# Performance work log

Hardware: AMD Instinct MI355X
Metric: run time of the kernel (lower is better)

## Reference

```python
import jax, jax.numpy as jnp
import numpy as np

N, N1, N2, K = 65536, 16384, 8192, 16
INDIM, HID, OUT = 64, 32, 128


def _knn_np(pos, q, k, chunk=1024):
    # brute-force chunked KNN (indices into pos) for setup only
    out = []
    for s in range(0, q.shape[0], chunk):
        d = ((q[s:s + chunk, None, :] - pos[None, :, :]) ** 2).sum(-1)
        out.append(np.argpartition(d, k, axis=1)[:, :k])
    return np.concatenate(out, 0)


def setup_inputs() -> dict:
    key = jax.random.key(0)
    ks = jax.random.split(key, 12)
    x = jax.random.normal(ks[0], (N, INDIM), jnp.float32)
    pos = jax.random.uniform(ks[1], (N, 3), jnp.float32)

    pos_np = np.asarray(pos)
    rng = np.random.default_rng(0)
    idx1 = np.sort(rng.choice(N, N1, replace=False))            # RandomSampler(ratio1)
    nn1 = _knn_np(pos_np, pos_np[idx1], K)                      # [N1, K] into full cloud
    src1, dst1 = nn1.reshape(-1), np.repeat(np.arange(N1), K)
    pos1 = pos_np[idx1]
    idx2 = np.sort(rng.choice(N1, N2, replace=False))           # RandomSampler(ratio2)
    nn2 = _knn_np(pos1, pos1[idx2], K)                          # [N2, K] into level-1 cloud
    src2, dst2 = nn2.reshape(-1), np.repeat(np.arange(N2), K)

    def lin(k, i, o):
        return jax.random.normal(k, (i, o), jnp.float32) / float(np.sqrt(i))

    return dict(
        x=x, pos=pos,
        W_down=lin(ks[2], INDIM, HID), b_down=jnp.zeros((HID,), jnp.float32),
        W_pp1=lin(ks[3], 10, 32), b_pp1=jnp.zeros((32,), jnp.float32),
        W_att1=lin(ks[4], 64, 64), b_att1=jnp.zeros((64,), jnp.float32),
        W_g1=lin(ks[5], 64, 64), b_g1=jnp.zeros((64,), jnp.float32),
        W_pp2=lin(ks[6], 10, 64), b_pp2=jnp.zeros((64,), jnp.float32),
        W_att2=lin(ks[7], 128, 128), b_att2=jnp.zeros((128,), jnp.float32),
        W_g2=lin(ks[8], 128, 128), b_g2=jnp.zeros((128,), jnp.float32),
        W_up=lin(ks[9], 128, OUT), b_up=jnp.zeros((OUT,), jnp.float32),
        W_sc=lin(ks[10], INDIM, OUT), b_sc=jnp.zeros((OUT,), jnp.float32),
        idx1=jnp.asarray(idx1, jnp.int32), idx2=jnp.asarray(idx2, jnp.int32),
        src1=jnp.asarray(src1, jnp.int32), dst1=jnp.asarray(dst1, jnp.int32),
        src2=jnp.asarray(src2, jnp.int32), dst2=jnp.asarray(dst2, jnp.int32),
    )


def _mlp(h, W, b):
    return jax.nn.relu(h @ W + b)


def _randla_conv(x, pos_all, pos_q, src, dst, Wpp, bpp, Watt, batt, Wg, bg, n_out):
    # RandlaKernel.message + add-aggregate + update (bipartite: targets = sampled points)
    pos_i, pos_j = pos_q[dst], pos_all[src]                     # [E,3]
    vij = pos_i - pos_j
    dij = jnp.sqrt((vij * vij).sum(-1, keepdims=True))          # [E,1]
    rel = jnp.concatenate([pos_i, pos_j, vij, dij], axis=1)     # [E,10]
    rij = _mlp(rel, Wpp, bpp)                                   # point_pos_nn
    fij = jnp.concatenate([x[src], rij], axis=1)                # [E, c+d]
    s = jax.nn.softmax(_mlp(fij, Watt, batt), axis=-1)          # softmax over feature dim (as in source)
    agg = jax.ops.segment_sum(s * fij, dst, num_segments=n_out) # aggr='add'
    return _mlp(agg, Wg, bg)                                    # global_nn


def reference(x, pos, W_down, b_down, W_pp1, b_pp1, W_att1, b_att1, W_g1, b_g1,
              W_pp2, b_pp2, W_att2, b_att2, W_g2, b_g2, W_up, b_up, W_sc, b_sc,
              idx1, idx2, src1, dst1, src2, dst2):
    h = _mlp(x, W_down, b_down)                                 # features_downsample (indim -> outdim//4)
    pos1 = pos[idx1]
    h = _randla_conv(h, pos, pos1, src1, dst1, W_pp1, b_pp1, W_att1, b_att1, W_g1, b_g1, N1)
    pos2 = pos1[idx2]
    h = _randla_conv(h, pos1, pos2, src2, dst2, W_pp2, b_pp2, W_att2, b_att2, W_g2, b_g2, N2)
    h = _mlp(h, W_up, b_up)                                     # features_upsample
    sc = _mlp(x[idx1][idx2], W_sc, b_sc)                        # shortcut resized, idx = idx1[idx2]
    return jax.nn.relu(h + sc)
```

## Files before the change

kernel.cpp:

```cpp
#include <hip/hip_runtime.h>

#define N_FULL 65536
#define NN1    16384
#define NN2    8192

typedef __attribute__((ext_vector_type(8))) short bf16x8;
typedef __attribute__((ext_vector_type(4))) float f32x4;
typedef unsigned short ushortT;

#define MFMA16(acc, a, b) acc = __builtin_amdgcn_mfma_f32_16x16x32_bf16(a, b, acc, 0, 0, 0)

static __device__ __forceinline__ ushortT f2bf(float f) {
    union { float f; unsigned u; } v; v.f = f;
    unsigned r = v.u + 0x7FFFu + ((v.u >> 16) & 1u);
    return (ushortT)(r >> 16);
}
static __device__ __forceinline__ unsigned pack2(float a, float b) {
    return (unsigned)f2bf(a) | ((unsigned)f2bf(b) << 16);
}
static __device__ __forceinline__ float bfu2f(ushortT h) {
    union { unsigned u; float f; } v; v.u = (unsigned)h << 16; return v.f;
}

#define WS_WDT   0
#define WS_WAT1  2304
#define WS_WGT1  6912
#define WS_WAT2  11520
#define WS_WGT2  28928
#define WS_WUPT  46336
#define WS_WSCT  63744
#define WS_H0    73728
#define WS_H1    (WS_H0 + 65536u*32u)
#define WS_AGG1  (WS_H1 + 16384u*64u)
#define WS_AGG2  (WS_AGG1 + 16384u*64u)

static __device__ __forceinline__ void tpose(
    const float* __restrict__ src, ushortT* __restrict__ dst,
    int K, int N, int STR, int gid, int gs)
{
    for (int i = gid; i < K * N; i += gs) {
        const int n = i / K, k = i - n * K;
        dst[n * STR + k] = f2bf(src[(size_t)k * N + n]);
    }
}

__global__ __launch_bounds__(256) void k_prep(
    const float* __restrict__ Wd, const float* __restrict__ Wa1,
    const float* __restrict__ Wg1, const float* __restrict__ Wa2,
    const float* __restrict__ Wg2, const float* __restrict__ Wup,
    const float* __restrict__ Wsc, ushortT* __restrict__ wsw)
{
    const int gid = blockIdx.x * 256 + threadIdx.x, gs = gridDim.x * 256;
    tpose(Wd,  wsw + WS_WDT,  64, 32, 72,  gid, gs);
    tpose(Wa1, wsw + WS_WAT1, 64, 64, 72,  gid, gs);
    tpose(Wg1, wsw + WS_WGT1, 64, 64, 72,  gid, gs);
    tpose(Wa2, wsw + WS_WAT2, 128, 128, 136, gid, gs);
    tpose(Wg2, wsw + WS_WGT2, 128, 128, 136, gid, gs);
    tpose(Wup, wsw + WS_WUPT, 128, 128, 136, gid, gs);
    tpose(Wsc, wsw + WS_WSCT, 64, 128, 72, gid, gs);
}

__global__ __launch_bounds__(256) void k_down(
    const float* __restrict__ x, const ushortT* __restrict__ wsw,
    const float* __restrict__ bd, ushortT* __restrict__ h0w)
{
    __shared__ ushortT Al[128 * 72];
    __shared__ ushortT Bl[32 * 72];
    const int t = threadIdx.x;
    const int rowBase = blockIdx.x * 128;

    {
        const int r = t >> 1, c0 = (t & 1) * 32;
        unsigned* dst = (unsigned*)Al + r * 36 + (c0 >> 1);
        const float* src = &x[(size_t)(rowBase + r) * 64 + c0];
#pragma unroll
        for (int j = 0; j < 32; j += 4) {
            const float4 v = *reinterpret_cast<const float4*>(src + j);
            dst[(j >> 1) + 0] = pack2(v.x, v.y);
            dst[(j >> 1) + 1] = pack2(v.z, v.w);
        }
        const unsigned* wsrc = (const unsigned*)(wsw + WS_WDT);
        for (int i = t; i < 1152; i += 256) ((unsigned*)Bl)[i] = wsrc[i];
    }
    __syncthreads();

    const int lane = t & 63, w = t >> 6, quad = lane >> 4, c16 = lane & 15;
    f32x4 acc[2][2];
#pragma unroll
    for (int mt = 0; mt < 2; ++mt)
#pragma unroll
        for (int nt = 0; nt < 2; ++nt)
#pragma unroll
            for (int r = 0; r < 4; ++r) acc[mt][nt][r] = 0.f;
#pragma unroll
    for (int ks = 0; ks < 2; ++ks) {
        bf16x8 a[2], b[2];
#pragma unroll
        for (int mt = 0; mt < 2; ++mt)
            a[mt] = *(const bf16x8*)&Al[(w * 32 + mt * 16 + c16) * 72 + ks * 32 + quad * 8];
#pragma unroll
        for (int nt = 0; nt < 2; ++nt)
            b[nt] = *(const bf16x8*)&Bl[(nt * 16 + c16) * 72 + ks * 32 + quad * 8];
#pragma unroll
        for (int mt = 0; mt < 2; ++mt)
#pragma unroll
            for (int nt = 0; nt < 2; ++nt) MFMA16(acc[mt][nt], a[mt], b[nt]);
    }
#pragma unroll
    for (int nt = 0; nt < 2; ++nt) {
        const int col = nt * 16 + c16;
        const float bias = bd[col];
#pragma unroll
        for (int mt = 0; mt < 2; ++mt)
#pragma unroll
            for (int r = 0; r < 4; ++r) {
                const int row = rowBase + w * 32 + mt * 16 + quad * 4 + r;
                h0w[(size_t)row * 32 + col] = f2bf(fmaxf(acc[mt][nt][r] + bias, 0.f));
            }
    }
}

__global__ __launch_bounds__(256) void k_conv1(
    const ushortT* __restrict__ h0w, const float* __restrict__ pos,
    const int* __restrict__ idx1, const int* __restrict__ src1,
    const float* __restrict__ Wpp, const float* __restrict__ bpp,
    const ushortT* __restrict__ wsw, const float* __restrict__ batt,
    ushortT* __restrict__ agg1w)
{
    __shared__ ushortT Fl[128 * 72];
    __shared__ ushortT Wl[64 * 72];
    __shared__ float Pl[352];
    const int t = threadIdx.x;
    const int d0 = blockIdx.x * 8;

    {
        const unsigned* wsrc = (const unsigned*)(wsw + WS_WAT1);
        for (int i = t; i < 2304; i += 256) ((unsigned*)Wl)[i] = wsrc[i];
        for (int i = t; i < 352; i += 256) Pl[i] = (i < 320) ? Wpp[i] : bpp[i - 320];
    }
    __syncthreads();

    {
        const int e = t >> 1, half = t & 1;
        const int g = e >> 4;
        const int s = src1[(d0 + g) * 16 + (e & 15)];
        const unsigned* srcp = (const unsigned*)h0w + (size_t)s * 16 + half * 8;
        unsigned* dstp = (unsigned*)Fl + e * 36 + half * 8;
#pragma unroll
        for (int j = 0; j < 8; ++j) dstp[j] = srcp[j];

        const int pin = idx1[d0 + g];
        const float pix = pos[pin * 3 + 0], piy = pos[pin * 3 + 1], piz = pos[pin * 3 + 2];
        const float pjx = pos[s * 3 + 0],  pjy = pos[s * 3 + 1],  pjz = pos[s * 3 + 2];
        const float vx = pix - pjx, vy = piy - pjy, vz = piz - pjz;
        const float dij = sqrtf(vx * vx + vy * vy + vz * vz);
        const float rel[10] = {pix, piy, piz, pjx, pjy, pjz, vx, vy, vz, dij};
        const int c0 = half * 16;
#pragma unroll
        for (int c = 0; c < 16; c += 2) {
            float a0 = Pl[320 + c0 + c], a1 = Pl[320 + c0 + c + 1];
#pragma unroll
            for (int i = 0; i < 10; ++i) {
                a0 += rel[i] * Pl[i * 32 + c0 + c];
                a1 += rel[i] * Pl[i * 32 + c0 + c + 1];
            }
            ((unsigned*)Fl)[(e * 72 + 32 + c0 + c) >> 1] = pack2(fmaxf(a0, 0.f), fmaxf(a1, 0.f));
        }
    }
    __syncthreads();

    const int lane = t & 63, w = t >> 6, quad = lane >> 4, c16 = lane & 15;
    f32x4 acc[2][4];
#pragma unroll
    for (int mt = 0; mt < 2; ++mt)
#pragma unroll
        for (int nt = 0; nt < 4; ++nt)
#pragma unroll
            for (int r = 0; r < 4; ++r) acc[mt][nt][r] = 0.f;
#pragma unroll
    for (int ks = 0; ks < 2; ++ks) {
        bf16x8 a[2], b[4];
#pragma unroll
        for (int mt = 0; mt < 2; ++mt)
            a[mt] = *(const bf16x8*)&Fl[(w * 32 + mt * 16 + c16) * 72 + ks * 32 + quad * 8];
#pragma unroll
        for (int nt = 0; nt < 4; ++nt)
            b[nt] = *(const bf16x8*)&Wl[(nt * 16 + c16) * 72 + ks * 32 + quad * 8];
#pragma unroll
        for (int mt = 0; mt < 2; ++mt)
#pragma unroll
            for (int nt = 0; nt < 4; ++nt) MFMA16(acc[mt][nt], a[mt], b[nt]);
    }
    float bcol[4];
#pragma unroll
    for (int nt = 0; nt < 4; ++nt) bcol[nt] = batt[nt * 16 + c16];

#pragma unroll
    for (int mt = 0; mt < 2; ++mt) {
#pragma unroll
        for (int nt = 0; nt < 4; ++nt)
#pragma unroll
            for (int r = 0; r < 4; ++r)
                acc[mt][nt][r] = fmaxf(acc[mt][nt][r] + bcol[nt], 0.f);
        float rs[4];
#pragma unroll
        for (int r = 0; r < 4; ++r) {
            float mx = acc[mt][0][r];
#pragma unroll
            for (int nt = 1; nt < 4; ++nt) mx = fmaxf(mx, acc[mt][nt][r]);
            mx = fmaxf(mx, __shfl_xor(mx, 1));
            mx = fmaxf(mx, __shfl_xor(mx, 2));
            mx = fmaxf(mx, __shfl_xor(mx, 4));
            mx = fmaxf(mx, __shfl_xor(mx, 8));
            float sm = 0.f;
#pragma unroll
            for (int nt = 0; nt < 4; ++nt) {
                acc[mt][nt][r] = __expf(acc[mt][nt][r] - mx);
                sm += acc[mt][nt][r];
            }
            sm += __shfl_xor(sm, 1);
            sm += __shfl_xor(sm, 2);
            sm += __shfl_xor(sm, 4);
            sm += __shfl_xor(sm, 8);
            rs[r] = 1.f / sm;
        }
#pragma unroll
        for (int nt = 0; nt < 4; ++nt) {
            float v = 0.f;
#pragma unroll
            for (int r = 0; r < 4; ++r) {
                const float fv = bfu2f(Fl[(w * 32 + mt * 16 + quad * 4 + r) * 72 + nt * 16 + c16]);
                v += acc[mt][nt][r] * rs[r] * fv;
            }
            v += __shfl_xor(v, 16);
            v += __shfl_xor(v, 32);
            if (lane < 16)
                agg1w[(size_t)(d0 + w * 2 + mt) * 64 + nt * 16 + c16] = f2bf(v);
        }
    }
}

__global__ __launch_bounds__(256) void k_gemm1(
    const ushortT* __restrict__ agg1w, const ushortT* __restrict__ wsw,
    const float* __restrict__ bg, ushortT* __restrict__ h1w)
{
    __shared__ ushortT Al[128 * 72];
    __shared__ ushortT Wl[64 * 72];
    const int t = threadIdx.x;
    const int d0 = blockIdx.x * 128;

    for (int i = t; i < 4096; i += 256) {
        const int r = i >> 5, j = i & 31;
        ((unsigned*)Al)[r * 36 + j] = ((const unsigned*)agg1w)[(size_t)(d0 + r) * 32 + j];
    }
    {
        const unsigned* wsrc = (const unsigned*)(wsw + WS_WGT1);
        for (int i = t; i < 2304; i += 256) ((unsigned*)Wl)[i] = wsrc[i];
    }
    __syncthreads();

    const int lane = t & 63, w = t >> 6, quad = lane >> 4, c16 = lane & 15;
    f32x4 acc[2][4];
#pragma unroll
    for (int mt = 0; mt < 2; ++mt)
#pragma unroll
        for (int nt = 0; nt < 4; ++nt)
#pragma unroll
            for (int r = 0; r < 4; ++r) acc[mt][nt][r] = 0.f;
#pragma unroll
    for (int ks = 0; ks < 2; ++ks) {
        bf16x8 a[2], b[4];
#pragma unroll
        for (int mt = 0; mt < 2; ++mt)
            a[mt] = *(const bf16x8*)&Al[(w * 32 + mt * 16 + c16) * 72 + ks * 32 + quad * 8];
#pragma unroll
        for (int nt = 0; nt < 4; ++nt)
            b[nt] = *(const bf16x8*)&Wl[(nt * 16 + c16) * 72 + ks * 32 + quad * 8];
#pragma unroll
        for (int mt = 0; mt < 2; ++mt)
#pragma unroll
            for (int nt = 0; nt < 4; ++nt) MFMA16(acc[mt][nt], a[mt], b[nt]);
    }
#pragma unroll
    for (int nt = 0; nt < 4; ++nt) {
        const int col = nt * 16 + c16;
        const float bias = bg[col];
#pragma unroll
        for (int mt = 0; mt < 2; ++mt)
#pragma unroll
            for (int r = 0; r < 4; ++r) {
                const int row = d0 + w * 32 + mt * 16 + quad * 4 + r;
                h1w[(size_t)row * 64 + col] = f2bf(fmaxf(acc[mt][nt][r] + bias, 0.f));
            }
    }
}

__global__ __launch_bounds__(256) void k_conv2(
    const ushortT* __restrict__ h1w, const float* __restrict__ pos,
    const int* __restrict__ idx1, const int* __restrict__ idx2,
    const int* __restrict__ src2,
    const float* __restrict__ Wpp, const float* __restrict__ bpp,
    const ushortT* __restrict__ wsw, const float* __restrict__ batt,
    ushortT* __restrict__ agg2w)
{
    __shared__ ushortT Fl[128 * 136];
    __shared__ ushortT Wl[128 * 136];
    __shared__ float Pl[704];
    const int t = threadIdx.x;
    const int d0 = blockIdx.x * 8;

    {
        const unsigned* wsrc = (const unsigned*)(wsw + WS_WAT2);
        for (int i = t; i < 8704; i += 256) ((unsigned*)Wl)[i] = wsrc[i];
        for (int i = t; i < 704; i += 256) Pl[i] = (i < 640) ? Wpp[i] : bpp[i - 640];
    }
    __syncthreads();

    {
        const int e = t >> 1, half = t & 1;
        const int g = e >> 4;
        const int s = src2[(d0 + g) * 16 + (e & 15)];
        const unsigned* srcp = (const unsigned*)h1w + (size_t)s * 32 + half * 16;
        unsigned* dstp = (unsigned*)Fl + e * 68 + half * 16;
#pragma unroll
        for (int j = 0; j < 16; ++j) dstp[j] = srcp[j];

        const int pin = idx1[idx2[d0 + g]];
        const int sn = idx1[s];
        const float pix = pos[pin * 3 + 0], piy = pos[pin * 3 + 1], piz = pos[pin * 3 + 2];
        const float pjx = pos[sn * 3 + 0],  pjy = pos[sn * 3 + 1],  pjz = pos[sn * 3 + 2];
        const float vx = pix - pjx, vy = piy - pjy, vz = piz - pjz;
        const float dij = sqrtf(vx * vx + vy * vy + vz * vz);
        const float rel[10] = {pix, piy, piz, pjx, pjy, pjz, vx, vy, vz, dij};
        const int c0 = half * 32;
#pragma unroll
        for (int c = 0; c < 32; c += 2) {
            float a0 = Pl[640 + c0 + c], a1 = Pl[640 + c0 + c + 1];
#pragma unroll
            for (int i = 0; i < 10; ++i) {
                a0 += rel[i] * Pl[i * 64 + c0 + c];
                a1 += rel[i] * Pl[i * 64 + c0 + c + 1];
            }
            ((unsigned*)Fl)[(e * 136 + 64 + c0 + c) >> 1] = pack2(fmaxf(a0, 0.f), fmaxf(a1, 0.f));
        }
    }
    __syncthreads();

    const int lane = t & 63, w = t >> 6, quad = lane >> 4, c16 = lane & 15;
    f32x4 acc[2][8];
#pragma unroll
    for (int mt = 0; mt < 2; ++mt)
#pragma unroll
        for (int nt = 0; nt < 8; ++nt)
#pragma unroll
            for (int r = 0; r < 4; ++r) acc[mt][nt][r] = 0.f;
#pragma unroll
    for (int ks = 0; ks < 4; ++ks) {
        bf16x8 a[2], b[8];
#pragma unroll
        for (int mt = 0; mt < 2; ++mt)
            a[mt] = *(const bf16x8*)&Fl[(w * 32 + mt * 16 + c16) * 136 + ks * 32 + quad * 8];
#pragma unroll
        for (int nt = 0; nt < 8; ++nt)
            b[nt] = *(const bf16x8*)&Wl[(nt * 16 + c16) * 136 + ks * 32 + quad * 8];
#pragma unroll
        for (int mt = 0; mt < 2; ++mt)
#pragma unroll
            for (int nt = 0; nt < 8; ++nt) MFMA16(acc[mt][nt], a[mt], b[nt]);
    }
    float bcol[8];
#pragma unroll
    for (int nt = 0; nt < 8; ++nt) bcol[nt] = batt[nt * 16 + c16];

#pragma unroll
    for (int mt = 0; mt < 2; ++mt) {
#pragma unroll
        for (int nt = 0; nt < 8; ++nt)
#pragma unroll
            for (int r = 0; r < 4; ++r)
                acc[mt][nt][r] = fmaxf(acc[mt][nt][r] + bcol[nt], 0.f);
        float rs[4];
#pragma unroll
        for (int r = 0; r < 4; ++r) {
            float mx = acc[mt][0][r];
#pragma unroll
            for (int nt = 1; nt < 8; ++nt) mx = fmaxf(mx, acc[mt][nt][r]);
            mx = fmaxf(mx, __shfl_xor(mx, 1));
            mx = fmaxf(mx, __shfl_xor(mx, 2));
            mx = fmaxf(mx, __shfl_xor(mx, 4));
            mx = fmaxf(mx, __shfl_xor(mx, 8));
            float sm = 0.f;
#pragma unroll
            for (int nt = 0; nt < 8; ++nt) {
                acc[mt][nt][r] = __expf(acc[mt][nt][r] - mx);
                sm += acc[mt][nt][r];
            }
            sm += __shfl_xor(sm, 1);
            sm += __shfl_xor(sm, 2);
            sm += __shfl_xor(sm, 4);
            sm += __shfl_xor(sm, 8);
            rs[r] = 1.f / sm;
        }
#pragma unroll
        for (int nt = 0; nt < 8; ++nt) {
            float v = 0.f;
#pragma unroll
            for (int r = 0; r < 4; ++r) {
                const float fv = bfu2f(Fl[(w * 32 + mt * 16 + quad * 4 + r) * 136 + nt * 16 + c16]);
                v += acc[mt][nt][r] * rs[r] * fv;
            }
            v += __shfl_xor(v, 16);
            v += __shfl_xor(v, 32);
            if (lane < 16)
                agg2w[(size_t)(d0 + w * 2 + mt) * 128 + nt * 16 + c16] = f2bf(v);
        }
    }
}

__global__ __launch_bounds__(256) void k_post(
    const ushortT* __restrict__ agg2w, const float* __restrict__ x,
    const int* __restrict__ idx1, const int* __restrict__ idx2,
    const ushortT* __restrict__ wsw,
    const float* __restrict__ bg, const float* __restrict__ bup,
    const float* __restrict__ bsc, float* __restrict__ out)
{
    __shared__ ushortT Al[64 * 136];
    __shared__ ushortT Wl[128 * 136];
    __shared__ ushortT Bl[64 * 136];
    __shared__ ushortT A2[64 * 72];
    const int t = threadIdx.x;
    const int d0 = blockIdx.x * 64;

    for (int i = t; i < 4096; i += 256) {
        const int r = i >> 6, j = i & 63;
        ((unsigned*)Al)[r * 68 + j] = ((const unsigned*)agg2w)[(size_t)(d0 + r) * 64 + j];
    }
    {
        const int r = t >> 2, q = t & 3;
        const int pin = idx1[idx2[d0 + r]];
        const float* src = &x[(size_t)pin * 64 + q * 16];
        unsigned* dst = (unsigned*)A2 + r * 36 + q * 8;
#pragma unroll
        for (int j = 0; j < 8; ++j) {
            const float2 v = *reinterpret_cast<const float2*>(src + j * 2);
            dst[j] = pack2(v.x, v.y);
        }
    }
    {
        const unsigned* wsrc = (const unsigned*)(wsw + WS_WGT2);
        for (int i = t; i < 8704; i += 256) ((unsigned*)Wl)[i] = wsrc[i];
    }
    __syncthreads();

    const int lane = t & 63, w = t >> 6, quad = lane >> 4, c16 = lane & 15;

    {
        f32x4 acc[8];
#pragma unroll
        for (int nt = 0; nt < 8; ++nt)
#pragma unroll
            for (int r = 0; r < 4; ++r) acc[nt][r] = 0.f;
#pragma unroll
        for (int ks = 0; ks < 4; ++ks) {
            const bf16x8 a = *(const bf16x8*)&Al[(w * 16 + c16) * 136 + ks * 32 + quad * 8];
#pragma unroll
            for (int nt = 0; nt < 8; ++nt) {
                const bf16x8 b = *(const bf16x8*)&Wl[(nt * 16 + c16) * 136 + ks * 32 + quad * 8];
                MFMA16(acc[nt], a, b);
            }
        }
#pragma unroll
        for (int nt = 0; nt < 8; ++nt) {
            const int col = nt * 16 + c16;
            const float bias = bg[col];
#pragma unroll
            for (int r = 0; r < 4; ++r)
                Bl[(w * 16 + quad * 4 + r) * 136 + col] = f2bf(fmaxf(acc[nt][r] + bias, 0.f));
        }
    }
    __syncthreads();
    {
        const unsigned* wsrc = (const unsigned*)(wsw + WS_WUPT);
        for (int i = t; i < 8704; i += 256) ((unsigned*)Wl)[i] = wsrc[i];
    }
    __syncthreads();

    f32x4 u[8];
    {
#pragma unroll
        for (int nt = 0; nt < 8; ++nt)
#pragma unroll
            for (int r = 0; r < 4; ++r) u[nt][r] = 0.f;
#pragma unroll
        for (int ks = 0; ks < 4; ++ks) {
            const bf16x8 a = *(const bf16x8*)&Bl[(w * 16 + c16) * 136 + ks * 32 + quad * 8];
#pragma unroll
            for (int nt = 0; nt < 8; ++nt) {
                const bf16x8 b = *(const bf16x8*)&Wl[(nt * 16 + c16) * 136 + ks * 32 + quad * 8];
                MFMA16(u[nt], a, b);
            }
        }
#pragma unroll
        for (int nt = 0; nt < 8; ++nt) {
            const float bias = bup[nt * 16 + c16];
#pragma unroll
            for (int r = 0; r < 4; ++r) u[nt][r] = fmaxf(u[nt][r] + bias, 0.f);
        }
    }
    __syncthreads();
    {
        const unsigned* wsrc = (const unsigned*)(wsw + WS_WSCT);
        for (int i = t; i < 4608; i += 256) ((unsigned*)Wl)[i] = wsrc[i];
    }
    __syncthreads();

    {
        f32x4 acc[8];
#pragma unroll
        for (int nt = 0; nt < 8; ++nt)
#pragma unroll
            for (int r = 0; r < 4; ++r) acc[nt][r] = 0.f;
        const ushortT* Wsc_l = Wl;
#pragma unroll
        for (int ks = 0; ks < 2; ++ks) {
            const bf16x8 a = *(const bf16x8*)&A2[(w * 16 + c16) * 72 + ks * 32 + quad * 8];
#pragma unroll
            for (int nt = 0; nt < 8; ++nt) {
                const bf16x8 b = *(const bf16x8*)&Wsc_l[(nt * 16 + c16) * 72 + ks * 32 + quad * 8];
                MFMA16(acc[nt], a, b);
            }
        }
#pragma unroll
        for (int nt = 0; nt < 8; ++nt) {
            const int col = nt * 16 + c16;
            const float bias = bsc[col];
#pragma unroll
            for (int r = 0; r < 4; ++r) {
                const float sc = fmaxf(acc[nt][r] + bias, 0.f);
                const int row = d0 + w * 16 + quad * 4 + r;
                out[(size_t)row * 128 + col] = u[nt][r] + sc;
            }
        }
    }
}

extern "C" void kernel_launch(void* const* d_in, const int* in_sizes, int n_in,
                              void* d_out, int out_size, void* d_ws, size_t ws_size,
                              hipStream_t stream)
{
    const float* x      = (const float*)d_in[0];
    const float* pos    = (const float*)d_in[1];
    const float* W_down = (const float*)d_in[2];
    const float* b_down = (const float*)d_in[3];
    const float* W_pp1  = (const float*)d_in[4];
    const float* b_pp1  = (const float*)d_in[5];
    const float* W_att1 = (const float*)d_in[6];
    const float* b_att1 = (const float*)d_in[7];
    const float* W_g1   = (const float*)d_in[8];
    const float* b_g1   = (const float*)d_in[9];
    const float* W_pp2  = (const float*)d_in[10];
    const float* b_pp2  = (const float*)d_in[11];
    const float* W_att2 = (const float*)d_in[12];
    const float* b_att2 = (const float*)d_in[13];
    const float* W_g2   = (const float*)d_in[14];
    const float* b_g2   = (const float*)d_in[15];
    const float* W_up   = (const float*)d_in[16];
    const float* b_up   = (const float*)d_in[17];
    const float* W_sc   = (const float*)d_in[18];
    const float* b_sc   = (const float*)d_in[19];
    const int* idx1 = (const int*)d_in[20];
    const int* idx2 = (const int*)d_in[21];
    const int* src1 = (const int*)d_in[22];
    const int* src2 = (const int*)d_in[24];

    ushortT* wsw = (ushortT*)d_ws;
    ushortT* h0w   = wsw + WS_H0;
    ushortT* h1w   = wsw + WS_H1;
    ushortT* agg1w = wsw + WS_AGG1;
    ushortT* agg2w = wsw + WS_AGG2;

    k_prep <<<68, 256, 0, stream>>>(W_down, W_att1, W_g1, W_att2, W_g2, W_up, W_sc, wsw);
    k_down <<<N_FULL / 128, 256, 0, stream>>>(x, wsw, b_down, h0w);
    k_conv1<<<NN1 / 8, 256, 0, stream>>>(h0w, pos, idx1, src1,
                                         W_pp1, b_pp1, wsw, b_att1, agg1w);
    k_gemm1<<<NN1 / 128, 256, 0, stream>>>(agg1w, wsw, b_g1, h1w);
    k_conv2<<<NN2 / 8, 256, 0, stream>>>(h1w, pos, idx1, idx2, src2,
                                         W_pp2, b_pp2, wsw, b_att2, agg2w);
    k_post <<<NN2 / 64, 256, 0, stream>>>(agg2w, x, idx1, idx2, wsw,
                                          b_g2, b_up, b_sc, (float*)d_out);
}
```

Before: 203.0 us.

## Fuse global_nn GEMM into conv1, vectorize loads, shrink post tiles

The level-1 global_nn GEMM moves into k_conv1: each block writes its 8 aggregated rows to a zero-padded 16-row LDS tile and applies W_g1 with one MFMA per wave. This removes the agg1 round trip through global memory and one kernel launch. Weight and gather copies are widened to uint4 loads. The sync after the weight loads is moved to overlap with the gather and position math. k_post is halved to 32 rows per block, giving more blocks but more redundant weight loads per row, and conv1 now uses extra LDS for W_g1.

```diff
diff --git a/kernel.cpp b/kernel.cpp
--- a/kernel.cpp
+++ b/kernel.cpp
@@ -31,8 +31,7 @@
 #define WS_WSCT  63744
 #define WS_H0    73728
 #define WS_H1    (WS_H0 + 65536u*32u)
-#define WS_AGG1  (WS_H1 + 16384u*64u)
-#define WS_AGG2  (WS_AGG1 + 16384u*64u)
+#define WS_AGG2  (WS_H1 + 16384u*64u)
 
 static __device__ __forceinline__ void tpose(
     const float* __restrict__ src, ushortT* __restrict__ dst,
@@ -64,8 +63,8 @@
     const float* __restrict__ x, const ushortT* __restrict__ wsw,
     const float* __restrict__ bd, ushortT* __restrict__ h0w)
 {
-    __shared__ ushortT Al[128 * 72];
-    __shared__ ushortT Bl[32 * 72];
+    __shared__ __align__(16) ushortT Al[128 * 72];
+    __shared__ __align__(16) ushortT Bl[32 * 72];
     const int t = threadIdx.x;
     const int rowBase = blockIdx.x * 128;
 
@@ -79,8 +78,9 @@
             dst[(j >> 1) + 0] = pack2(v.x, v.y);
             dst[(j >> 1) + 1] = pack2(v.z, v.w);
         }
-        const unsigned* wsrc = (const unsigned*)(wsw + WS_WDT);
-        for (int i = t; i < 1152; i += 256) ((unsigned*)Bl)[i] = wsrc[i];
+        const uint4* wsrc = (const uint4*)(wsw + WS_WDT);
+        uint4* bl4 = (uint4*)Bl;
+        for (int i = t; i < 288; i += 256) bl4[i] = wsrc[i];
     }
     __syncthreads();
 
@@ -125,29 +125,34 @@
     const int* __restrict__ idx1, const int* __restrict__ src1,
     const float* __restrict__ Wpp, const float* __restrict__ bpp,
     const ushortT* __restrict__ wsw, const float* __restrict__ batt,
-    ushortT* __restrict__ agg1w)
-{
-    __shared__ ushortT Fl[128 * 72];
-    __shared__ ushortT Wl[64 * 72];
+    const float* __restrict__ bg, ushortT* __restrict__ h1w)
+{
+    __shared__ __align__(16) ushortT Fl[128 * 72];
+    __shared__ __align__(16) ushortT Wl[64 * 72];
+    __shared__ __align__(16) ushortT Gl[64 * 72];
+    __shared__ __align__(16) ushortT A2ls[16 * 72];
     __shared__ float Pl[352];
     const int t = threadIdx.x;
     const int d0 = blockIdx.x * 8;
 
     {
-        const unsigned* wsrc = (const unsigned*)(wsw + WS_WAT1);
-        for (int i = t; i < 2304; i += 256) ((unsigned*)Wl)[i] = wsrc[i];
+        const uint4* wa = (const uint4*)(wsw + WS_WAT1);
+        const uint4* wg = (const uint4*)(wsw + WS_WGT1);
+        uint4* wl4 = (uint4*)Wl;
+        uint4* gl4 = (uint4*)Gl;
+        for (int i = t; i < 576; i += 256) { wl4[i] = wa[i]; gl4[i] = wg[i]; }
         for (int i = t; i < 352; i += 256) Pl[i] = (i < 320) ? Wpp[i] : bpp[i - 320];
-    }
-    __syncthreads();
+        for (int i = t; i < 288; i += 256) ((unsigned*)A2ls)[288 + i] = 0;
+    }
 
     {
         const int e = t >> 1, half = t & 1;
         const int g = e >> 4;
         const int s = src1[(d0 + g) * 16 + (e & 15)];
-        const unsigned* srcp = (const unsigned*)h0w + (size_t)s * 16 + half * 8;
-        unsigned* dstp = (unsigned*)Fl + e * 36 + half * 8;
-#pragma unroll
-        for (int j = 0; j < 8; ++j) dstp[j] = srcp[j];
+        const uint4* srcp = (const uint4*)((const unsigned*)h0w + (size_t)s * 16 + half * 8);
+        uint4* dstp = (uint4*)((unsigned*)Fl + e * 36 + half * 8);
+        dstp[0] = srcp[0];
+        dstp[1] = srcp[1];
 
         const int pin = idx1[d0 + g];
         const float pix = pos[pin * 3 + 0], piy = pos[pin * 3 + 1], piz = pos[pin * 3 + 2];
@@ -155,6 +160,7 @@
         const float vx = pix - pjx, vy = piy - pjy, vz = piz - pjz;
         const float dij = sqrtf(vx * vx + vy * vy + vz * vz);
         const float rel[10] = {pix, piy, piz, pjx, pjy, pjz, vx, vy, vz, dij};
+        __syncthreads();
         const int c0 = half * 16;
 #pragma unroll
         for (int c = 0; c < 16; c += 2) {
@@ -235,63 +241,28 @@
             v += __shfl_xor(v, 16);
             v += __shfl_xor(v, 32);
             if (lane < 16)
-                agg1w[(size_t)(d0 + w * 2 + mt) * 64 + nt * 16 + c16] = f2bf(v);
-        }
-    }
-}
-
-__global__ __launch_bounds__(256) void k_gemm1(
-    const ushortT* __restrict__ agg1w, const ushortT* __restrict__ wsw,
-    const float* __restrict__ bg, ushortT* __restrict__ h1w)
-{
-    __shared__ ushortT Al[128 * 72];
-    __shared__ ushortT Wl[64 * 72];
-    const int t = threadIdx.x;
-    const int d0 = blockIdx.x * 128;
-
-    for (int i = t; i < 4096; i += 256) {
-        const int r = i >> 5, j = i & 31;
-        ((unsigned*)Al)[r * 36 + j] = ((const unsigned*)agg1w)[(size_t)(d0 + r) * 32 + j];
-    }
-    {
-        const unsigned* wsrc = (const unsigned*)(wsw + WS_WGT1);
-        for (int i = t; i < 2304; i += 256) ((unsigned*)Wl)[i] = wsrc[i];
-    }
-    __syncthreads();
-
-    const int lane = t & 63, w = t >> 6, quad = lane >> 4, c16 = lane & 15;
-    f32x4 acc[2][4];
-#pragma unroll
-    for (int mt = 0; mt < 2; ++mt)
-#pragma unroll
-        for (int nt = 0; nt < 4; ++nt)
-#pragma unroll
-            for (int r = 0; r < 4; ++r) acc[mt][nt][r] = 0.f;
-#pragma unroll
-    for (int ks = 0; ks < 2; ++ks) {
-        bf16x8 a[2], b[4];
-#pragma unroll
-        for (int mt = 0; mt < 2; ++mt)
-            a[mt] = *(const bf16x8*)&Al[(w * 32 + mt * 16 + c16) * 72 + ks * 32 + quad * 8];
-#pragma unroll
-        for (int nt = 0; nt < 4; ++nt)
-            b[nt] = *(const bf16x8*)&Wl[(nt * 16 + c16) * 72 + ks * 32 + quad * 8];
-#pragma unroll
-        for (int mt = 0; mt < 2; ++mt)
-#pragma unroll
-            for (int nt = 0; nt < 4; ++nt) MFMA16(acc[mt][nt], a[mt], b[nt]);
-    }
-#pragma unroll
-    for (int nt = 0; nt < 4; ++nt) {
-        const int col = nt * 16 + c16;
+                A2ls[(w * 2 + mt) * 72 + nt * 16 + c16] = f2bf(v);
+        }
+    }
+    __syncthreads();
+
+    {
+        f32x4 acc2 = {0.f, 0.f, 0.f, 0.f};
+#pragma unroll
+        for (int ks = 0; ks < 2; ++ks) {
+            const bf16x8 a = *(const bf16x8*)&A2ls[c16 * 72 + ks * 32 + quad * 8];
+            const bf16x8 b = *(const bf16x8*)&Gl[(w * 16 + c16) * 72 + ks * 32 + quad * 8];
+            MFMA16(acc2, a, b);
+        }
+        const int col = w * 16 + c16;
         const float bias = bg[col];
-#pragma unroll
-        for (int mt = 0; mt < 2; ++mt)
+        if (quad < 2) {
 #pragma unroll
             for (int r = 0; r < 4; ++r) {
-                const int row = d0 + w * 32 + mt * 16 + quad * 4 + r;
-                h1w[(size_t)row * 64 + col] = f2bf(fmaxf(acc[mt][nt][r] + bias, 0.f));
-            }
+                const int row = quad * 4 + r;
+                h1w[(size_t)(d0 + row) * 64 + col] = f2bf(fmaxf(acc2[r] + bias, 0.f));
+            }
+        }
     }
 }
 
@@ -303,27 +274,27 @@
     const ushortT* __restrict__ wsw, const float* __restrict__ batt,
     ushortT* __restrict__ agg2w)
 {
-    __shared__ ushortT Fl[128 * 136];
-    __shared__ ushortT Wl[128 * 136];
+    __shared__ __align__(16) ushortT Fl[128 * 136];
+    __shared__ __align__(16) ushortT Wl[128 * 136];
     __shared__ float Pl[704];
     const int t = threadIdx.x;
     const int d0 = blockIdx.x * 8;
 
     {
-        const unsigned* wsrc = (const unsigned*)(wsw + WS_WAT2);
-        for (int i = t; i < 8704; i += 256) ((unsigned*)Wl)[i] = wsrc[i];
+        const uint4* wsrc = (const uint4*)(wsw + WS_WAT2);
+        uint4* wl4 = (uint4*)Wl;
+        for (int i = t; i < 2176; i += 256) wl4[i] = wsrc[i];
         for (int i = t; i < 704; i += 256) Pl[i] = (i < 640) ? Wpp[i] : bpp[i - 640];
     }
-    __syncthreads();
 
     {
         const int e = t >> 1, half = t & 1;
         const int g = e >> 4;
         const int s = src2[(d0 + g) * 16 + (e & 15)];
-        const unsigned* srcp = (const unsigned*)h1w + (size_t)s * 32 + half * 16;
-        unsigned* dstp = (unsigned*)Fl + e * 68 + half * 16;
-#pragma unroll
-        for (int j = 0; j < 16; ++j) dstp[j] = srcp[j];
+        const uint4* srcp = (const uint4*)((const unsigned*)h1w + (size_t)s * 32 + half * 16);
+        uint4* dstp = (uint4*)((unsigned*)Fl + e * 68 + half * 16);
+#pragma unroll
+        for (int j = 0; j < 4; ++j) dstp[j] = srcp[j];
 
         const int pin = idx1[idx2[d0 + g]];
         const int sn = idx1[s];
@@ -332,6 +303,7 @@
         const float vx = pix - pjx, vy = piy - pjy, vz = piz - pjz;
         const float dij = sqrtf(vx * vx + vy * vy + vz * vz);
         const float rel[10] = {pix, piy, piz, pjx, pjy, pjz, vx, vy, vz, dij};
+        __syncthreads();
         const int c0 = half * 32;
 #pragma unroll
         for (int c = 0; c < 32; c += 2) {
@@ -424,120 +396,125 @@
     const float* __restrict__ bg, const float* __restrict__ bup,
     const float* __restrict__ bsc, float* __restrict__ out)
 {
-    __shared__ ushortT Al[64 * 136];
-    __shared__ ushortT Wl[128 * 136];
-    __shared__ ushortT Bl[64 * 136];
-    __shared__ ushortT A2[64 * 72];
+    __shared__ __align__(16) ushortT Al[32 * 136];
+    __shared__ __align__(16) ushortT Wl[128 * 136];
+    __shared__ __align__(16) ushortT Bl[32 * 136];
+    __shared__ __align__(16) ushortT A2[32 * 72];
     const int t = threadIdx.x;
-    const int d0 = blockIdx.x * 64;
-
-    for (int i = t; i < 4096; i += 256) {
-        const int r = i >> 6, j = i & 63;
-        ((unsigned*)Al)[r * 68 + j] = ((const unsigned*)agg2w)[(size_t)(d0 + r) * 64 + j];
-    }
-    {
-        const int r = t >> 2, q = t & 3;
+    const int d0 = blockIdx.x * 32;
+
+    for (int i = t; i < 512; i += 256) {
+        const int r = i >> 4, j = i & 15;
+        ((uint4*)((unsigned*)Al + r * 68))[j] =
+            ((const uint4*)((const unsigned*)agg2w + (size_t)(d0 + r) * 64))[j];
+    }
+    {
+        const int r = t >> 3, q = t & 7;
         const int pin = idx1[idx2[d0 + r]];
-        const float* src = &x[(size_t)pin * 64 + q * 16];
-        unsigned* dst = (unsigned*)A2 + r * 36 + q * 8;
-#pragma unroll
-        for (int j = 0; j < 8; ++j) {
+        const float* src = &x[(size_t)pin * 64 + q * 8];
+        unsigned* dst = (unsigned*)A2 + r * 36 + q * 4;
+#pragma unroll
+        for (int j = 0; j < 4; ++j) {
             const float2 v = *reinterpret_cast<const float2*>(src + j * 2);
             dst[j] = pack2(v.x, v.y);
         }
     }
     {
-        const unsigned* wsrc = (const unsigned*)(wsw + WS_WGT2);
-        for (int i = t; i < 8704; i += 256) ((unsigned*)Wl)[i] = wsrc[i];
+        const uint4* wsrc = (const uint4*)(wsw + WS_WGT2);
+        uint4* wl4 = (uint4*)Wl;
+        for (int i = t; i < 2176; i += 256) wl4[i] = wsrc[i];
     }
     __syncthreads();
 
     const int lane = t & 63, w = t >> 6, quad = lane >> 4, c16 = lane & 15;
-
-    {
-        f32x4 acc[8];
-#pragma unroll
-        for (int nt = 0; nt < 8; ++nt)
+    const int mtw = w >> 1;
+    const int ntb = (w & 1) * 4;
+
+    {
+        f32x4 acc[4];
+#pragma unroll
+        for (int nt = 0; nt < 4; ++nt)
 #pragma unroll
             for (int r = 0; r < 4; ++r) acc[nt][r] = 0.f;
 #pragma unroll
         for (int ks = 0; ks < 4; ++ks) {
-            const bf16x8 a = *(const bf16x8*)&Al[(w * 16 + c16) * 136 + ks * 32 + quad * 8];
-#pragma unroll
-            for (int nt = 0; nt < 8; ++nt) {
-                const bf16x8 b = *(const bf16x8*)&Wl[(nt * 16 + c16) * 136 + ks * 32 + quad * 8];
+            const bf16x8 a = *(const bf16x8*)&Al[(mtw * 16 + c16) * 136 + ks * 32 + quad * 8];
+#pragma unroll
+            for (int nt = 0; nt < 4; ++nt) {
+                const bf16x8 b = *(const bf16x8*)&Wl[((ntb + nt) * 16 + c16) * 136 + ks * 32 + quad * 8];
                 MFMA16(acc[nt], a, b);
             }
         }
 #pragma unroll
-        for (int nt = 0; nt < 8; ++nt) {
-            const int col = nt * 16 + c16;
+        for (int nt = 0; nt < 4; ++nt) {
+            const int col = (ntb + nt) * 16 + c16;
             const float bias = bg[col];
 #pragma unroll
             for (int r = 0; r < 4; ++r)
-                Bl[(w * 16 + quad * 4 + r) * 136 + col] = f2bf(fmaxf(acc[nt][r] + bias, 0.f));
-        }
-    }
-    __syncthreads();
-    {
-        const unsigned* wsrc = (const unsigned*)(wsw + WS_WUPT);
-        for (int i = t; i < 8704; i += 256) ((unsigned*)Wl)[i] = wsrc[i];
-    }
-    __syncthreads();
-
-    f32x4 u[8];
-    {
-#pragma unroll
-        for (int nt = 0; nt < 8; ++nt)
+                Bl[(mtw * 16 + quad * 4 + r) * 136 + col] = f2bf(fmaxf(acc[nt][r] + bias, 0.f));
+        }
+    }
+    __syncthreads();
+    {
+        const uint4* wsrc = (const uint4*)(wsw + WS_WUPT);
+        uint4* wl4 = (uint4*)Wl;
+        for (int i = t; i < 2176; i += 256) wl4[i] = wsrc[i];
+    }
+    __syncthreads();
+
+    f32x4 u[4];
+    {
+#pragma unroll
+        for (int nt = 0; nt < 4; ++nt)
 #pragma unroll
             for (int r = 0; r < 4; ++r) u[nt][r] = 0.f;
 #pragma unroll
         for (int ks = 0; ks < 4; ++ks) {
-            const bf16x8 a = *(const bf16x8*)&Bl[(w * 16 + c16) * 136 + ks * 32 + quad * 8];
-#pragma unroll
-            for (int nt = 0; nt < 8; ++nt) {
-                const bf16x8 b = *(const bf16x8*)&Wl[(nt * 16 + c16) * 136 + ks * 32 + quad * 8];
+            const bf16x8 a = *(const bf16x8*)&Bl[(mtw * 16 + c16) * 136 + ks * 32 + quad * 8];
+#pragma unroll
+            for (int nt = 0; nt < 4; ++nt) {
+                const bf16x8 b = *(const bf16x8*)&Wl[((ntb + nt) * 16 + c16) * 136 + ks * 32 + quad * 8];
                 MFMA16(u[nt], a, b);
             }
         }
 #pragma unroll
-        for (int nt = 0; nt < 8; ++nt) {
-            const float bias = bup[nt * 16 + c16];
+        for (int nt = 0; nt < 4; ++nt) {
+            const float bias = bup[(ntb + nt) * 16 + c16];
 #pragma unroll
             for (int r = 0; r < 4; ++r) u[nt][r] = fmaxf(u[nt][r] + bias, 0.f);
         }
     }
     __syncthreads();
     {
-        const unsigned* wsrc = (const unsigned*)(wsw + WS_WSCT);
-        for (int i = t; i < 4608; i += 256) ((unsigned*)Wl)[i] = wsrc[i];
-    }
-    __syncthreads();
-
-    {
-        f32x4 acc[8];
-#pragma unroll
-        for (int nt = 0; nt < 8; ++nt)
+        const uint4* wsrc = (const uint4*)(wsw + WS_WSCT);
+        uint4* wl4 = (uint4*)Wl;
+        for (int i = t; i < 1152; i += 256) wl4[i] = wsrc[i];
+    }
+    __syncthreads();
+
+    {
+        f32x4 acc[4];
+#pragma unroll
+        for (int nt = 0; nt < 4; ++nt)
 #pragma unroll
             for (int r = 0; r < 4; ++r) acc[nt][r] = 0.f;
-        const ushortT* Wsc_l = Wl;
 #pragma unroll
         for (int ks = 0; ks < 2; ++ks) {
-            const bf16x8 a = *(const bf16x8*)&A2[(w * 16 + c16) * 72 + ks * 32 + quad * 8];
-#pragma unroll
-            for (int nt = 0; nt < 8; ++nt) {
-                const bf16x8 b = *(const bf16x8*)&Wsc_l[(nt * 16 + c16) * 72 + ks * 32 + quad * 8];
+            const bf16x8 a = *(const bf16x8*)&A2[(mtw * 16 + c16) * 72 + ks * 32 + quad * 8];
+#pragma unroll
+            for (int nt = 0; nt < 4; ++nt) {
+                const bf16x8 b = *(const bf16x8*)&Wl[((ntb + nt) * 16 + c16) * 72 + ks * 32 + quad * 8];
                 MFMA16(acc[nt], a, b);
             }
         }
 #pragma unroll
-        for (int nt = 0; nt < 8; ++nt) {
-            const int col = nt * 16 + c16;
+        for (int nt = 0; nt < 4; ++nt) {
+            const int col = (ntb + nt) * 16 + c16;
             const float bias = bsc[col];
 #pragma unroll
             for (int r = 0; r < 4; ++r) {
                 const float sc = fmaxf(acc[nt][r] + bias, 0.f);
-                const int row = d0 + w * 16 + quad * 4 + r;
+                const int row = d0 + mtw * 16 + quad * 4 + r;
                 out[(size_t)row * 128 + col] = u[nt][r] + sc;
             }
         }
@@ -576,16 +553,14 @@
     ushortT* wsw = (ushortT*)d_ws;
     ushortT* h0w   = wsw + WS_H0;
     ushortT* h1w   = wsw + WS_H1;
-    ushortT* agg1w = wsw + WS_AGG1;
     ushortT* agg2w = wsw + WS_AGG2;
 
     k_prep <<<68, 256, 0, stream>>>(W_down, W_att1, W_g1, W_att2, W_g2, W_up, W_sc, wsw);
     k_down <<<N_FULL / 128, 256, 0, stream>>>(x, wsw, b_down, h0w);
     k_conv1<<<NN1 / 8, 256, 0, stream>>>(h0w, pos, idx1, src1,
-                                         W_pp1, b_pp1, wsw, b_att1, agg1w);
-    k_gemm1<<<NN1 / 128, 256, 0, stream>>>(agg1w, wsw, b_g1, h1w);
+                                         W_pp1, b_pp1, wsw, b_att1, b_g1, h1w);
     k_conv2<<<NN2 / 8, 256, 0, stream>>>(h1w, pos, idx1, idx2, src2,
                                          W_pp2, b_pp2, wsw, b_att2, agg2w);
-    k_post <<<NN2 / 64, 256, 0, stream>>>(agg2w, x, idx1, idx2, wsw,
+    k_post <<<NN2 / 32, 256, 0, stream>>>(agg2w, x, idx1, idx2, wsw,
                                           b_g2, b_up, b_sc, (float*)d_out);
 }
```

After: 183.4 us. 9.6% less time.
